# Optimization experiments

Hardware: AMD Instinct MI355X
Metric: run time of the kernel (lower is better)

## Reference

```python
import jax, jax.numpy as jnp
import numpy as np

NUM_HEADS = 16
HEAD_DIM = 64
HIDDEN = NUM_HEADS * HEAD_DIM  # 1024
SEQ_LEN = 4096


def setup_inputs() -> dict:
    key = jax.random.key(0)
    ks = jax.random.split(key, 8)
    hidden_states = jax.random.normal(ks[0], (SEQ_LEN, HIDDEN), dtype=jnp.float32)
    cu_seqlens = jnp.sort(jax.random.randint(ks[1], (5,), 0, SEQ_LEN)).astype(jnp.int32)
    cos = jax.random.uniform(ks[2], (SEQ_LEN, HEAD_DIM), dtype=jnp.float32)
    sin = jax.random.uniform(ks[3], (SEQ_LEN, HEAD_DIM), dtype=jnp.float32)
    W_qkv = jax.random.normal(ks[4], (HIDDEN, 3 * HIDDEN), dtype=jnp.float32) * 0.02
    b_qkv = jax.random.normal(ks[5], (3 * HIDDEN,), dtype=jnp.float32) * 0.02
    W_proj = jax.random.normal(ks[6], (HIDDEN, HIDDEN), dtype=jnp.float32) * 0.02
    b_proj = jax.random.normal(ks[7], (HIDDEN,), dtype=jnp.float32) * 0.02
    return {
        "hidden_states": hidden_states,
        "cu_seqlens": cu_seqlens,
        "cos": cos,
        "sin": sin,
        "W_qkv": W_qkv,
        "b_qkv": b_qkv,
        "W_proj": W_proj,
        "b_proj": b_proj,
    }


def _rotate_half(x):
    x1, x2 = jnp.split(x, 2, axis=-1)
    return jnp.concatenate([-x2, x1], axis=-1)


def reference(hidden_states, cu_seqlens, cos, sin, W_qkv, b_qkv, W_proj, b_proj):
    # NOTE: original module does not use cu_seqlens for masking (full dense attention).
    seq_len = hidden_states.shape[0]
    qkv = hidden_states @ W_qkv + b_qkv  # (S, 3*H)
    qkv = qkv.reshape(seq_len, 3, NUM_HEADS, HEAD_DIM)
    q, k, v = qkv[:, 0], qkv[:, 1], qkv[:, 2]  # (S, nh, hd)
    c = cos[:, None, :]
    s = sin[:, None, :]
    q = q * c + _rotate_half(q) * s
    k = k * c + _rotate_half(k) * s
    scale = 1.0 / jnp.sqrt(jnp.float32(HEAD_DIM))
    # (nh, S, hd)
    q = q.transpose(1, 0, 2)
    k = k.transpose(1, 0, 2)
    v = v.transpose(1, 0, 2)
    attn = jnp.einsum('hqd,hkd->hqk', q, k) * scale
    attn = jax.nn.softmax(attn, axis=-1)
    out = jnp.einsum('hqk,hkd->hqd', attn, v)
    out = out.transpose(1, 0, 2).reshape(seq_len, HIDDEN)
    return out @ W_proj + b_proj
```

## Files before the change

### kernel.cpp

```cpp
#include <hip/hip_runtime.h>
#include <type_traits>

typedef short bf16x8 __attribute__((ext_vector_type(8)));
typedef float f32x4  __attribute__((ext_vector_type(4)));
typedef unsigned short u16;

#define MFMA(a,b,c) __builtin_amdgcn_mfma_f32_16x16x32_bf16((a),(b),(c),0,0,0)

__device__ __forceinline__ float bf2f(u16 u){ unsigned x=((unsigned)u)<<16; return __builtin_bit_cast(float,x); }
__device__ __forceinline__ u16 f2bf(float f){ unsigned x=__builtin_bit_cast(unsigned,f); x += 0x7fffu + ((x>>16)&1u); return (u16)(x>>16); }
__device__ __forceinline__ unsigned pkbf(float a, float b){
  unsigned ua = __builtin_bit_cast(unsigned, a), ub = __builtin_bit_cast(unsigned, b);
  ua += 0x7fffu + ((ua>>16)&1u);
  ub += 0x7fffu + ((ub>>16)&1u);
  return __builtin_amdgcn_perm(ub, ua, 0x07060302u);
}
__device__ __forceinline__ void async_cp16(const u16* g, u16* l){
  __builtin_amdgcn_global_load_lds((const __attribute__((address_space(1))) void*)g,
                                   (__attribute__((address_space(3))) void*)l, 16, 0, 0);
}

__global__ __launch_bounds__(256) void cvt_f32_bf16(const float* __restrict__ in, u16* __restrict__ out, int n){
  int i = (blockIdx.x*256 + threadIdx.x)*4;
  if (i >= n) return;
  float4 v = *(const float4*)(in + i);
  ushort4 o;
  o.x = f2bf(v.x); o.y = f2bf(v.y); o.z = f2bf(v.z); o.w = f2bf(v.w);
  *(ushort4*)(out + i) = o;
}

__global__ __launch_bounds__(256) void transpose_f32_bf16(const float* __restrict__ in, u16* __restrict__ out, int R, int C){
  __shared__ u16 tile[32][33];
  int bc = blockIdx.x*32, br = blockIdx.y*32;
  int tx = threadIdx.x & 31, ty = threadIdx.x >> 5;
  #pragma unroll
  for (int i=ty;i<32;i+=8) tile[i][tx] = f2bf(in[(size_t)(br+i)*C + bc + tx]);
  __syncthreads();
  #pragma unroll
  for (int i=ty;i<32;i+=8) out[(size_t)(bc+i)*R + br + tx] = tile[tx][i];
}

__global__ __launch_bounds__(256) void vtrans_perm_bf16(const u16* __restrict__ in, u16* __restrict__ out){
  __shared__ u16 tile[32][33];
  const int h = blockIdx.z;
  const u16* ip = in + (size_t)h*4096*64;
  u16* op = out + (size_t)h*64*4096;
  int bt = blockIdx.x*32, bd = blockIdx.y*32;
  int tx = threadIdx.x & 31, ty = threadIdx.x >> 5;
  #pragma unroll
  for (int i=ty;i<32;i+=8) tile[i][tx] = ip[(size_t)(bt+i)*64 + bd + tx];
  __syncthreads();
  const int tlog = ((tx>>2)&1)*16 + (tx>>3)*4 + (tx&3);
  #pragma unroll
  for (int i=ty;i<32;i+=8) op[(size_t)(bd+i)*4096 + bt + tx] = tile[tlog][i];
}

template<int BN, typename OutT>
__global__ __launch_bounds__(256) void gemm_bt_bias(
    const u16* __restrict__ A, const u16* __restrict__ Bt,
    const float* __restrict__ bias, OutT* __restrict__ C,
    int M, int N, int K)
{
  __shared__ __align__(16) u16 As[128*32];
  __shared__ __align__(16) u16 Bs[BN*32];
  const int m0 = blockIdx.y*128, n0 = blockIdx.x*BN;
  const int tid = threadIdx.x;
  const int wave = tid>>6, lane = tid&63;
  const int wr = (wave>>1)*64, wc = (wave&1)*(BN/2);
  const int ml = lane&15, quad = lane>>4;
  const int lrow = lane>>2;
  const int scol = ((lane&3) ^ (lrow&3))*8;
  const int rsw  = (quad ^ (ml&3))*8;
  const u16* gA0 = A + (size_t)(m0 + wave*32      + lrow)*K + scol;
  const u16* gA1 = A + (size_t)(m0 + wave*32 + 16 + lrow)*K + scol;
  u16* lA0 = &As[wave*1024];
  u16* lA1 = &As[wave*1024 + 512];
  constexpr int BI = BN/64;
  const u16* gB[BI]; u16* lB[BI];
  #pragma unroll
  for (int t=0;t<BI;t++){
    gB[t] = Bt + (size_t)(n0 + (wave*BI+t)*16 + lrow)*K + scol;
    lB[t] = &Bs[(wave*BI+t)*512];
  }
  constexpr int NJ = BN/32;
  f32x4 acc[4][NJ] = {};
  for (int k0=0; k0<K; k0+=32) {
    async_cp16(gA0 + k0, lA0);
    async_cp16(gA1 + k0, lA1);
    #pragma unroll
    for (int t=0;t<BI;t++) async_cp16(gB[t] + k0, lB[t]);
    __syncthreads();
    bf16x8 af[4], bfr[NJ];
    #pragma unroll
    for (int i=0;i<4;i++)  af[i]  = *(const bf16x8*)&As[(wr+i*16+ml)*32 + rsw];
    #pragma unroll
    for (int j=0;j<NJ;j++) bfr[j] = *(const bf16x8*)&Bs[(wc+j*16+ml)*32 + rsw];
    #pragma unroll
    for (int i=0;i<4;i++)
      #pragma unroll
      for (int j=0;j<NJ;j++)
        acc[i][j] = MFMA(af[i], bfr[j], acc[i][j]);
    __syncthreads();
  }
  #pragma unroll
  for (int j=0;j<NJ;j++){
    int col = n0 + wc + j*16 + ml;
    float bv = bias[col];
    #pragma unroll
    for (int i=0;i<4;i++){
      int row0 = m0 + wr + i*16 + quad*4;
      #pragma unroll
      for (int r=0;r<4;r++){
        float val = acc[i][j][r] + bv;
        if constexpr (std::is_same_v<OutT, float>)
          C[(size_t)(row0+r)*N + col] = val;
        else
          C[(size_t)(row0+r)*N + col] = f2bf(val);
      }
    }
  }
}

__global__ __launch_bounds__(256) void rope_split(
    const u16* __restrict__ QKV, const float* __restrict__ cosb, const float* __restrict__ sinb,
    u16* __restrict__ Qo, u16* __restrict__ Ko, u16* __restrict__ Vo)
{
  const int t = blockIdx.x;
  const int d = threadIdx.x & 63;
  const int h0 = threadIdx.x >> 6;
  const float cv = cosb[t*64+d];
  const float sv = sinb[t*64+d];
  const int dp = (d<32) ? d+32 : d-32;
  const float sgn = (d<32) ? -1.f : 1.f;
  #pragma unroll
  for (int h=h0; h<16; h+=4) {
    const u16* base = QKV + (size_t)t*3072 + h*64;
    float q  = bf2f(base[d]);
    float k  = bf2f(base[1024+d]);
    float v  = bf2f(base[2048+d]);
    float qp = bf2f(base[dp]);
    float kp = bf2f(base[1024+dp]);
    float qr = q*cv + sgn*qp*sv;
    float kr = k*cv + sgn*kp*sv;
    Qo[((size_t)h*4096 + t)*64 + d] = f2bf(qr*(0.125f*1.44269504f));
    Ko[((size_t)h*4096 + t)*64 + d] = f2bf(kr);
    Vo[((size_t)h*4096 + t)*64 + d] = f2bf(v);
  }
}

__global__ __launch_bounds__(256,4) void flash_attn(
    const u16* __restrict__ Q, const u16* __restrict__ Kg, const u16* __restrict__ VT,
    u16* __restrict__ Opart, float* __restrict__ Lpart)
{
  constexpr int SEQ=4096, HALF=2048;
  __shared__ __align__(16) u16 Ks[64*64];
  __shared__ __align__(16) u16 Vs[64*64];
  const int qt=blockIdx.x, h=blockIdx.y, ks=blockIdx.z;
  const int tid=threadIdx.x, wave=tid>>6, lane=tid&63;
  const int ml=lane&15, quad=lane>>4;
  const int qbase = qt*128 + wave*32;
  bf16x8 qf[2][2];
  #pragma unroll
  for (int qi=0; qi<2; qi++){
    const u16* qp = Q + ((size_t)h*SEQ + qbase + qi*16 + ml)*64;
    qf[qi][0] = *(const bf16x8*)(qp + quad*8);
    qf[qi][1] = *(const bf16x8*)(qp + 32 + quad*8);
  }
  const bf16x8 ones = {0x3F80,0x3F80,0x3F80,0x3F80,0x3F80,0x3F80,0x3F80,0x3F80};
  f32x4 o[2][4] = {};
  f32x4 accsum[2] = {};
  const int lrow8 = lane>>3, lchk = lane&7;
  const int swzg = (lchk ^ lrow8)*8;
  const u16* kgl = Kg + (size_t)h*SEQ*64 + (size_t)(ks*HALF + wave*16 + lrow8)*64 + swzg;
  const u16* vgl = VT + (size_t)h*64*SEQ + (size_t)(wave*16 + lrow8)*SEQ + ks*HALF + swzg;
  u16* kl0 = &Ks[(wave*16  )*64];
  u16* kl1 = &Ks[(wave*16+8)*64];
  u16* vl0 = &Vs[(wave*16  )*64];
  u16* vl1 = &Vs[(wave*16+8)*64];
  const int swzA = (quad     ^ (ml&7))*8;
  const int swzB = ((quad^4) ^ (ml&7))*8;

  for (int k0=0;k0<HALF;k0+=64) {
    async_cp16(kgl + (size_t)k0*64,       kl0);
    async_cp16(kgl + (size_t)k0*64 + 512, kl1);
    async_cp16(vgl + k0,                  vl0);
    async_cp16(vgl + 8*SEQ + k0,          vl1);
    __syncthreads();
    bf16x8 vf[4][2];
    #pragma unroll
    for (int db=0;db<4;db++){
      vf[db][0] = *(const bf16x8*)&Vs[(db*16+ml)*64 + (( (quad  ) ^ (ml&7))*8)];
      vf[db][1] = *(const bf16x8*)&Vs[(db*16+ml)*64 + (( (quad|4) ^ (ml&7))*8)];
    }
    #pragma unroll
    for (int qi=0; qi<2; qi++){
      f32x4 s[4];
      #pragma unroll
      for (int kb=0;kb<4;kb++){
        bf16x8 kf0 = *(const bf16x8*)&Ks[(kb*16+ml)*64 + swzA];
        bf16x8 kf1 = *(const bf16x8*)&Ks[(kb*16+ml)*64 + swzB];
        f32x4 z = {0,0,0,0};
        z = MFMA(kf0, qf[qi][0], z);
        s[kb] = MFMA(kf1, qf[qi][1], z);
      }
      #pragma unroll
      for (int p=0;p<2;p++){
        float e0 = exp2f(s[2*p][0]),   e1 = exp2f(s[2*p][1]);
        float e2 = exp2f(s[2*p][2]),   e3 = exp2f(s[2*p][3]);
        float e4 = exp2f(s[2*p+1][0]), e5 = exp2f(s[2*p+1][1]);
        float e6 = exp2f(s[2*p+1][2]), e7 = exp2f(s[2*p+1][3]);
        union { uint4 u; bf16x8 v; } pf;
        pf.u.x = pkbf(e0,e1); pf.u.y = pkbf(e2,e3);
        pf.u.z = pkbf(e4,e5); pf.u.w = pkbf(e6,e7);
        accsum[qi] = MFMA(ones, pf.v, accsum[qi]);
        #pragma unroll
        for (int db=0;db<4;db++)
          o[qi][db] = MFMA(vf[db][p], pf.v, o[qi][db]);
      }
    }
    __syncthreads();
  }
  u16* op = Opart + (size_t)ks*4096*1024;
  #pragma unroll
  for (int qi=0;qi<2;qi++){
    size_t rb = (size_t)(qbase + qi*16 + ml)*1024 + h*64;
    #pragma unroll
    for (int db=0;db<4;db++){
      uint2 w;
      w.x = pkbf(o[qi][db][0], o[qi][db][1]);
      w.y = pkbf(o[qi][db][2], o[qi][db][3]);
      *(uint2*)&op[rb + db*16 + quad*4] = w;
    }
  }
  if (quad==0){
    float* lp = Lpart + (size_t)ks*16*4096 + (size_t)h*4096 + qbase;
    lp[ml]    = accsum[0][0];
    lp[16+ml] = accsum[1][0];
  }
}

__global__ __launch_bounds__(256) void combine_softmax(
    const u16* __restrict__ O0, const u16* __restrict__ O1,
    const float* __restrict__ L0, const float* __restrict__ L1,
    u16* __restrict__ AO)
{
  int i = (blockIdx.x*256 + threadIdx.x)*4;
  int row = i >> 10, col = i & 1023, h = col >> 6;
  float inv = 1.f/(L0[h*4096 + row] + L1[h*4096 + row]);
  ushort4 a = *(const ushort4*)(O0+i);
  ushort4 b = *(const ushort4*)(O1+i);
  ushort4 o;
  o.x = f2bf((bf2f(a.x)+bf2f(b.x))*inv);
  o.y = f2bf((bf2f(a.y)+bf2f(b.y))*inv);
  o.z = f2bf((bf2f(a.z)+bf2f(b.z))*inv);
  o.w = f2bf((bf2f(a.w)+bf2f(b.w))*inv);
  *(ushort4*)(AO+i) = o;
}

extern "C" void kernel_launch(void* const* d_in, const int* in_sizes, int n_in,
                              void* d_out, int out_size, void* d_ws, size_t ws_size,
                              hipStream_t stream)
{
  (void)in_sizes; (void)n_in; (void)out_size; (void)ws_size;
  const float* H     = (const float*)d_in[0];
  const float* cosb  = (const float*)d_in[2];
  const float* sinb  = (const float*)d_in[3];
  const float* Wqkv  = (const float*)d_in[4];
  const float* bqkv  = (const float*)d_in[5];
  const float* Wproj = (const float*)d_in[6];
  const float* bproj = (const float*)d_in[7];
  float* out = (float*)d_out;
  char* ws = (char*)d_ws;
  u16*   WqkvT  = (u16*)(ws + 0);
  float* Lpart  = (float*)(ws + 0);
  u16*   WprojT = (u16*)(ws + 6291456);
  u16*   Hb     = (u16*)(ws + 8388608);
  u16*   AO     = (u16*)(ws + 8388608);
  u16*   QKVr   = (u16*)(ws + 16777216);
  u16*   VTb    = (u16*)(ws + 16777216);
  u16*   Opart  = (u16*)(ws + 25165824);
  u16*   Qb     = (u16*)(ws + 41943040);
  u16*   Kb     = (u16*)(ws + 50331648);
  u16*   Vb     = (u16*)(ws + 58720256);

  hipLaunchKernelGGL(cvt_f32_bf16, dim3(4096), dim3(256), 0, stream, H, Hb, 4096*1024);
  hipLaunchKernelGGL(transpose_f32_bf16, dim3(96,32), dim3(256), 0, stream, Wqkv, WqkvT, 1024, 3072);
  hipLaunchKernelGGL(transpose_f32_bf16, dim3(32,32), dim3(256), 0, stream, Wproj, WprojT, 1024, 1024);
  hipLaunchKernelGGL((gemm_bt_bias<128,u16>), dim3(24,32), dim3(256), 0, stream, Hb, WqkvT, bqkv, QKVr, 4096, 3072, 1024);
  hipLaunchKernelGGL(rope_split, dim3(4096), dim3(256), 0, stream, QKVr, cosb, sinb, Qb, Kb, Vb);
  hipLaunchKernelGGL(vtrans_perm_bf16, dim3(128,2,16), dim3(256), 0, stream, Vb, VTb);
  hipLaunchKernelGGL(flash_attn, dim3(32,16,2), dim3(256), 0, stream, Qb, Kb, VTb, Opart, Lpart);
  hipLaunchKernelGGL(combine_softmax, dim3(4096), dim3(256), 0, stream,
                     Opart, Opart + (size_t)4096*1024, Lpart, Lpart + 16*4096, AO);
  hipLaunchKernelGGL((gemm_bt_bias<64,float>), dim3(16,32), dim3(256), 0, stream, AO, WprojT, bproj, out, 4096, 1024, 1024);
}
```

Baseline: 279.4 us.

## Split attention keys four ways and use hardware exp2 and bf16 pack

Raises the flash attention key split from two to four partitions, so the grid grows from 1024 to 2048 blocks and each block walks 1024 keys. The combine kernel now sums four partial outputs and denominators. The workspace layout is reshuffled to alias the extra partial buffers onto dead regions. It also switches to the hardware exp2 and packed bf16 conversion builtins and computes both query sub-tiles' scores before the PV loop. In exchange it adds partial-buffer traffic and a heavier combine step.

```diff
diff --git a/kernel.cpp b/kernel.cpp
--- a/kernel.cpp
+++ b/kernel.cpp
@@ -9,12 +9,28 @@
 
 __device__ __forceinline__ float bf2f(u16 u){ unsigned x=((unsigned)u)<<16; return __builtin_bit_cast(float,x); }
 __device__ __forceinline__ u16 f2bf(float f){ unsigned x=__builtin_bit_cast(unsigned,f); x += 0x7fffu + ((x>>16)&1u); return (u16)(x>>16); }
+
+#if __has_builtin(__builtin_amdgcn_cvt_pk_bf16_f32)
+typedef __bf16 hwbf2 __attribute__((ext_vector_type(2)));
+__device__ __forceinline__ unsigned pkbf(float a, float b){
+  hwbf2 r = __builtin_amdgcn_cvt_pk_bf16_f32(a, b);
+  return __builtin_bit_cast(unsigned, r);
+}
+#else
 __device__ __forceinline__ unsigned pkbf(float a, float b){
   unsigned ua = __builtin_bit_cast(unsigned, a), ub = __builtin_bit_cast(unsigned, b);
   ua += 0x7fffu + ((ua>>16)&1u);
   ub += 0x7fffu + ((ub>>16)&1u);
   return __builtin_amdgcn_perm(ub, ua, 0x07060302u);
 }
+#endif
+
+#if __has_builtin(__builtin_amdgcn_exp2f)
+#define EXP2(x) __builtin_amdgcn_exp2f(x)
+#else
+#define EXP2(x) exp2f(x)
+#endif
+
 __device__ __forceinline__ void async_cp16(const u16* g, u16* l){
   __builtin_amdgcn_global_load_lds((const __attribute__((address_space(1))) void*)g,
                                    (__attribute__((address_space(3))) void*)l, 16, 0, 0);
@@ -150,9 +166,10 @@
 
 __global__ __launch_bounds__(256,4) void flash_attn(
     const u16* __restrict__ Q, const u16* __restrict__ Kg, const u16* __restrict__ VT,
-    u16* __restrict__ Opart, float* __restrict__ Lpart)
-{
-  constexpr int SEQ=4096, HALF=2048;
+    u16* __restrict__ O0, u16* __restrict__ O1, u16* __restrict__ O2, u16* __restrict__ O3,
+    float* __restrict__ Lpart)
+{
+  constexpr int SEQ=4096, QTR=1024;
   __shared__ __align__(16) u16 Ks[64*64];
   __shared__ __align__(16) u16 Vs[64*64];
   const int qt=blockIdx.x, h=blockIdx.y, ks=blockIdx.z;
@@ -171,8 +188,8 @@
   f32x4 accsum[2] = {};
   const int lrow8 = lane>>3, lchk = lane&7;
   const int swzg = (lchk ^ lrow8)*8;
-  const u16* kgl = Kg + (size_t)h*SEQ*64 + (size_t)(ks*HALF + wave*16 + lrow8)*64 + swzg;
-  const u16* vgl = VT + (size_t)h*64*SEQ + (size_t)(wave*16 + lrow8)*SEQ + ks*HALF + swzg;
+  const u16* kgl = Kg + (size_t)h*SEQ*64 + (size_t)(ks*QTR + wave*16 + lrow8)*64 + swzg;
+  const u16* vgl = VT + (size_t)h*64*SEQ + (size_t)(wave*16 + lrow8)*SEQ + ks*QTR + swzg;
   u16* kl0 = &Ks[(wave*16  )*64];
   u16* kl1 = &Ks[(wave*16+8)*64];
   u16* vl0 = &Vs[(wave*16  )*64];
@@ -180,35 +197,35 @@
   const int swzA = (quad     ^ (ml&7))*8;
   const int swzB = ((quad^4) ^ (ml&7))*8;
 
-  for (int k0=0;k0<HALF;k0+=64) {
+  for (int k0=0;k0<QTR;k0+=64) {
     async_cp16(kgl + (size_t)k0*64,       kl0);
     async_cp16(kgl + (size_t)k0*64 + 512, kl1);
     async_cp16(vgl + k0,                  vl0);
     async_cp16(vgl + 8*SEQ + k0,          vl1);
     __syncthreads();
+    f32x4 s[2][4];
+    #pragma unroll
+    for (int kb=0;kb<4;kb++){
+      bf16x8 kf0 = *(const bf16x8*)&Ks[(kb*16+ml)*64 + swzA];
+      bf16x8 kf1 = *(const bf16x8*)&Ks[(kb*16+ml)*64 + swzB];
+      f32x4 z0={0,0,0,0}, z1={0,0,0,0};
+      z0 = MFMA(kf0, qf[0][0], z0); s[0][kb] = MFMA(kf1, qf[0][1], z0);
+      z1 = MFMA(kf0, qf[1][0], z1); s[1][kb] = MFMA(kf1, qf[1][1], z1);
+    }
     bf16x8 vf[4][2];
     #pragma unroll
     for (int db=0;db<4;db++){
-      vf[db][0] = *(const bf16x8*)&Vs[(db*16+ml)*64 + (( (quad  ) ^ (ml&7))*8)];
-      vf[db][1] = *(const bf16x8*)&Vs[(db*16+ml)*64 + (( (quad|4) ^ (ml&7))*8)];
+      vf[db][0] = *(const bf16x8*)&Vs[(db*16+ml)*64 + swzA];
+      vf[db][1] = *(const bf16x8*)&Vs[(db*16+ml)*64 + swzB];
     }
     #pragma unroll
-    for (int qi=0; qi<2; qi++){
-      f32x4 s[4];
-      #pragma unroll
-      for (int kb=0;kb<4;kb++){
-        bf16x8 kf0 = *(const bf16x8*)&Ks[(kb*16+ml)*64 + swzA];
-        bf16x8 kf1 = *(const bf16x8*)&Ks[(kb*16+ml)*64 + swzB];
-        f32x4 z = {0,0,0,0};
-        z = MFMA(kf0, qf[qi][0], z);
-        s[kb] = MFMA(kf1, qf[qi][1], z);
-      }
+    for (int qi=0; qi<2; qi++)
       #pragma unroll
       for (int p=0;p<2;p++){
-        float e0 = exp2f(s[2*p][0]),   e1 = exp2f(s[2*p][1]);
-        float e2 = exp2f(s[2*p][2]),   e3 = exp2f(s[2*p][3]);
-        float e4 = exp2f(s[2*p+1][0]), e5 = exp2f(s[2*p+1][1]);
-        float e6 = exp2f(s[2*p+1][2]), e7 = exp2f(s[2*p+1][3]);
+        float e0 = EXP2(s[qi][2*p][0]),   e1 = EXP2(s[qi][2*p][1]);
+        float e2 = EXP2(s[qi][2*p][2]),   e3 = EXP2(s[qi][2*p][3]);
+        float e4 = EXP2(s[qi][2*p+1][0]), e5 = EXP2(s[qi][2*p+1][1]);
+        float e6 = EXP2(s[qi][2*p+1][2]), e7 = EXP2(s[qi][2*p+1][3]);
         union { uint4 u; bf16x8 v; } pf;
         pf.u.x = pkbf(e0,e1); pf.u.y = pkbf(e2,e3);
         pf.u.z = pkbf(e4,e5); pf.u.w = pkbf(e6,e7);
@@ -217,10 +234,9 @@
         for (int db=0;db<4;db++)
           o[qi][db] = MFMA(vf[db][p], pf.v, o[qi][db]);
       }
-    }
     __syncthreads();
   }
-  u16* op = Opart + (size_t)ks*4096*1024;
+  u16* op = (ks==0) ? O0 : (ks==1) ? O1 : (ks==2) ? O2 : O3;
   #pragma unroll
   for (int qi=0;qi<2;qi++){
     size_t rb = (size_t)(qbase + qi*16 + ml)*1024 + h*64;
@@ -233,27 +249,30 @@
     }
   }
   if (quad==0){
-    float* lp = Lpart + (size_t)ks*16*4096 + (size_t)h*4096 + qbase;
+    float* lp = Lpart + (size_t)ks*65536 + (size_t)h*4096 + qbase;
     lp[ml]    = accsum[0][0];
     lp[16+ml] = accsum[1][0];
   }
 }
 
-__global__ __launch_bounds__(256) void combine_softmax(
+__global__ __launch_bounds__(256) void combine_softmax4(
     const u16* __restrict__ O0, const u16* __restrict__ O1,
-    const float* __restrict__ L0, const float* __restrict__ L1,
-    u16* __restrict__ AO)
+    const u16* __restrict__ O2, const u16* __restrict__ O3,
+    const float* __restrict__ L, u16* __restrict__ AO)
 {
   int i = (blockIdx.x*256 + threadIdx.x)*4;
   int row = i >> 10, col = i & 1023, h = col >> 6;
-  float inv = 1.f/(L0[h*4096 + row] + L1[h*4096 + row]);
+  int li = h*4096 + row;
+  float inv = 1.f/(L[li] + L[li+65536] + L[li+2*65536] + L[li+3*65536]);
   ushort4 a = *(const ushort4*)(O0+i);
   ushort4 b = *(const ushort4*)(O1+i);
+  ushort4 c = *(const ushort4*)(O2+i);
+  ushort4 d = *(const ushort4*)(O3+i);
   ushort4 o;
-  o.x = f2bf((bf2f(a.x)+bf2f(b.x))*inv);
-  o.y = f2bf((bf2f(a.y)+bf2f(b.y))*inv);
-  o.z = f2bf((bf2f(a.z)+bf2f(b.z))*inv);
-  o.w = f2bf((bf2f(a.w)+bf2f(b.w))*inv);
+  o.x = f2bf((bf2f(a.x)+bf2f(b.x)+bf2f(c.x)+bf2f(d.x))*inv);
+  o.y = f2bf((bf2f(a.y)+bf2f(b.y)+bf2f(c.y)+bf2f(d.y))*inv);
+  o.z = f2bf((bf2f(a.z)+bf2f(b.z)+bf2f(c.z)+bf2f(d.z))*inv);
+  o.w = f2bf((bf2f(a.w)+bf2f(b.w)+bf2f(c.w)+bf2f(d.w))*inv);
   *(ushort4*)(AO+i) = o;
 }
 
@@ -271,17 +290,20 @@
   const float* bproj = (const float*)d_in[7];
   float* out = (float*)d_out;
   char* ws = (char*)d_ws;
-  u16*   WqkvT  = (u16*)(ws + 0);
   float* Lpart  = (float*)(ws + 0);
-  u16*   WprojT = (u16*)(ws + 6291456);
-  u16*   Hb     = (u16*)(ws + 8388608);
-  u16*   AO     = (u16*)(ws + 8388608);
-  u16*   QKVr   = (u16*)(ws + 16777216);
-  u16*   VTb    = (u16*)(ws + 16777216);
-  u16*   Opart  = (u16*)(ws + 25165824);
-  u16*   Qb     = (u16*)(ws + 41943040);
-  u16*   Kb     = (u16*)(ws + 50331648);
-  u16*   Vb     = (u16*)(ws + 58720256);
+  u16*   WprojT = (u16*)(ws + 2097152);
+  u16*   Hb     = (u16*)(ws + 4194304);
+  u16*   Opart2 = (u16*)(ws + 4194304);
+  u16*   QKVr   = (u16*)(ws + 12582912);
+  u16*   VTb    = (u16*)(ws + 12582912);
+  u16*   Opart0 = (u16*)(ws + 20971520);
+  u16*   Opart1 = (u16*)(ws + 29360128);
+  u16*   WqkvT  = (u16*)(ws + 37748736);
+  u16*   Qb     = (u16*)(ws + 37748736);
+  u16*   AO     = (u16*)(ws + 37748736);
+  u16*   Kb     = (u16*)(ws + 46137344);
+  u16*   Vb     = (u16*)(ws + 54525952);
+  u16*   Opart3 = (u16*)(ws + 54525952);
 
   hipLaunchKernelGGL(cvt_f32_bf16, dim3(4096), dim3(256), 0, stream, H, Hb, 4096*1024);
   hipLaunchKernelGGL(transpose_f32_bf16, dim3(96,32), dim3(256), 0, stream, Wqkv, WqkvT, 1024, 3072);
@@ -289,8 +311,9 @@
   hipLaunchKernelGGL((gemm_bt_bias<128,u16>), dim3(24,32), dim3(256), 0, stream, Hb, WqkvT, bqkv, QKVr, 4096, 3072, 1024);
   hipLaunchKernelGGL(rope_split, dim3(4096), dim3(256), 0, stream, QKVr, cosb, sinb, Qb, Kb, Vb);
   hipLaunchKernelGGL(vtrans_perm_bf16, dim3(128,2,16), dim3(256), 0, stream, Vb, VTb);
-  hipLaunchKernelGGL(flash_attn, dim3(32,16,2), dim3(256), 0, stream, Qb, Kb, VTb, Opart, Lpart);
-  hipLaunchKernelGGL(combine_softmax, dim3(4096), dim3(256), 0, stream,
-                     Opart, Opart + (size_t)4096*1024, Lpart, Lpart + 16*4096, AO);
+  hipLaunchKernelGGL(flash_attn, dim3(32,16,4), dim3(256), 0, stream, Qb, Kb, VTb,
+                     Opart0, Opart1, Opart2, Opart3, Lpart);
+  hipLaunchKernelGGL(combine_softmax4, dim3(4096), dim3(256), 0, stream,
+                     Opart0, Opart1, Opart2, Opart3, Lpart, AO);
   hipLaunchKernelGGL((gemm_bt_bias<64,float>), dim3(16,32), dim3(256), 0, stream, AO, WprojT, bproj, out, 4096, 1024, 1024);
 }
```

New measurement: 256.3 us. 1.09x faster.
